# Performance work log

Measured on AMD Instinct MI355X. Metric: run time of the kernel, lower is better.

Reference implementation:

```python
import jax, jax.numpy as jnp
import numpy as np

D = 768
H = 12
HD = D // H
EPS = 1e-8  # torch cosine_similarity default eps


def setup_inputs() -> dict:
    key = jax.random.key(0)
    ks = jax.random.split(key, 16)
    bs, T, K = 8, 2048, 512
    s = 0.02
    return {
        "hidden_states": jax.random.normal(ks[0], (bs, T, D), jnp.float32),
        "attention_mask": jnp.ones((bs, T), jnp.int32),
        "pooled_hidden_states": jax.random.normal(ks[1], (bs, D), jnp.float32),
        "kg_key": jax.random.normal(ks[2], (bs, K, D), jnp.float32),
        "kg_value": jax.random.normal(ks[3], (bs, K, D), jnp.float32),
        "beta": jnp.ones((H,), jnp.float32),
        "Wq": jax.random.normal(ks[4], (D, D), jnp.float32) * s,
        "bq": jnp.zeros((D,), jnp.float32),
        "Wk": jax.random.normal(ks[5], (D, D), jnp.float32) * s,
        "bk": jnp.zeros((D,), jnp.float32),
        "Wv": jax.random.normal(ks[6], (D, D), jnp.float32) * s,
        "bv": jnp.zeros((D,), jnp.float32),
        "Wo": jax.random.normal(ks[7], (D, D), jnp.float32) * s,
        "bo": jnp.zeros((D,), jnp.float32),
    }


def reference(hidden_states, attention_mask, pooled_hidden_states, kg_key, kg_value,
              beta, Wq, bq, Wk, bk, Wv, bv, Wo, bo):
    bs, T, _ = hidden_states.shape
    K = kg_key.shape[1]
    # cosine similarity between pooled state and each KG key: [bs, K]
    pn = pooled_hidden_states / jnp.maximum(
        jnp.linalg.norm(pooled_hidden_states, axis=-1, keepdims=True), EPS)
    kn = kg_key / jnp.maximum(jnp.linalg.norm(kg_key, axis=-1, keepdims=True), EPS)
    sim = jnp.einsum("bd,bkd->bk", pn, kn)

    scale = HD ** -0.5
    # projections (torch Linear: y = x @ W.T + b)
    q = ((hidden_states @ Wq.T + bq) * scale).reshape(bs, T, H, HD).transpose(0, 2, 1, 3)
    k = (kg_value @ Wk.T + bk).reshape(bs, K, H, HD).transpose(0, 2, 1, 3)
    v = (kg_value @ Wv.T + bv).reshape(bs, K, H, HD).transpose(0, 2, 1, 3)

    # scores + per-head cosine-sim bias: [bs, H, T, K]
    scores = jnp.einsum("bhtd,bhkd->bhtk", q, k)
    scores = scores + beta[None, :, None, None] * sim[:, None, None, :]
    probs = jax.nn.softmax(scores, axis=-1)

    out = jnp.einsum("bhtk,bhkd->bhtd", probs, v)
    out = out.transpose(0, 2, 1, 3).reshape(bs, T, D)
    return out @ Wo.T + bo
```

## Files before the change

kernel.cpp:

```cpp
#include <hip/hip_runtime.h>
#include <math.h>

#define D_MODEL 768
#define NHEAD   12
#define HD      64
#define SEQ_T   2048
#define SEQ_K   512
#define BS      8
#define EPS_COS 1e-8f
#define LOG2E   1.44269504f

typedef short  bf16x8 __attribute__((ext_vector_type(8)));
typedef float  f32x4  __attribute__((ext_vector_type(4)));

__device__ __forceinline__ ushort f2bf(float x) {
    unsigned b = __float_as_uint(x);
    return (ushort)((b + 0x7FFF + ((b >> 16) & 1)) >> 16);
}
__device__ __forceinline__ unsigned cvt_pk_bf16(float lo, float hi) {
    unsigned r;
    asm("v_cvt_pk_bf16_f32 %0, %1, %2" : "=v"(r) : "v"(lo), "v"(hi));
    return r;
}
__device__ __forceinline__ float exp2_fast(float x) {
    float r;
    asm("v_exp_f32 %0, %1" : "=v"(r) : "v"(x));
    return r;
}

__device__ __forceinline__ void async_copy16(void* lds_base, const void* g_src) {
    __builtin_amdgcn_global_load_lds(
        (const __attribute__((address_space(1))) unsigned int*)g_src,
        (__attribute__((address_space(3))) unsigned int*)lds_base,
        16, 0, 0);
}

__global__ __launch_bounds__(256) void cvt4_kernel(
    const float* __restrict__ s0, const float* __restrict__ s1,
    const float* __restrict__ s2, const float* __restrict__ s3,
    ushort* __restrict__ d0, ushort* __restrict__ d1,
    ushort* __restrict__ d2, ushort* __restrict__ d3)
{
    const float* s; ushort* d;
    switch (blockIdx.y) {
        case 0: s = s0; d = d0; break;
        case 1: s = s1; d = d1; break;
        case 2: s = s2; d = d2; break;
        default: s = s3; d = d3; break;
    }
    int i = blockIdx.x * 256 + threadIdx.x;
    float4 v = reinterpret_cast<const float4*>(s)[i];
    ushort4 o;
    o.x = f2bf(v.x); o.y = f2bf(v.y); o.z = f2bf(v.z); o.w = f2bf(v.w);
    reinterpret_cast<ushort4*>(d)[i] = o;
}

__global__ __launch_bounds__(256) void sim_kernel(
    const float* __restrict__ pooled, const float* __restrict__ kg_key,
    const float* __restrict__ beta, float* __restrict__ bsim)
{
    int wid  = (blockIdx.x * blockDim.x + threadIdx.x) >> 6;
    int lane = threadIdx.x & 63;
    int b  = wid >> 9;
    int kk = wid & 511;
    const float* p   = pooled + (size_t)b * D_MODEL;
    const float* key = kg_key + ((size_t)b * SEQ_K + kk) * D_MODEL;
    float dpk = 0.f, dkk = 0.f, dpp = 0.f;
    for (int i = lane; i < D_MODEL; i += 64) {
        float pv = p[i], kv = key[i];
        dpk += pv * kv; dkk += kv * kv; dpp += pv * pv;
    }
    for (int off = 32; off; off >>= 1) {
        dpk += __shfl_xor(dpk, off);
        dkk += __shfl_xor(dkk, off);
        dpp += __shfl_xor(dpp, off);
    }
    if (lane == 0) {
        float np_ = fmaxf(sqrtf(dpp), EPS_COS);
        float nk_ = fmaxf(sqrtf(dkk), EPS_COS);
        float sv = (dpk / (np_ * nk_)) * LOG2E;
#pragma unroll
        for (int h = 0; h < NHEAD; ++h)
            bsim[(size_t)(b * NHEAD + h) * SEQ_K + kk] = beta[h] * sv;
    }
}

__global__ __launch_bounds__(256, 3) void gemm_q_a32_kernel(
    const float* __restrict__ A, const ushort* __restrict__ W,
    const float* __restrict__ bias, ushort* __restrict__ out_bf, float scale)
{
    constexpr int Kd = D_MODEL;
    __shared__ __align__(16) float  AsF[128 * 64];
    __shared__ __align__(16) ushort Bs[128 * 64];
    const int tid = threadIdx.x, wid = tid >> 6, l = tid & 63;
    const int g = l >> 4, c = l & 15;
    const int m0 = blockIdx.x * 128, n0 = blockIdx.y * 128;
    const int wm = (wid >> 1) * 64, wn = (wid & 1) * 64;

    f32x4 acc[4][4] = {};

    for (int k0 = 0; k0 < Kd; k0 += 64) {
        __syncthreads();
#pragma unroll
        for (int it = 0; it < 8; ++it) {
            int L = wid * 8192 + it * 1024 + l * 16;
            int row = L >> 8;
            int blk = (L >> 4) & 15;
            int gb = (blk & 8) | ((blk & 7) ^ (row & 7));
            async_copy16((char*)AsF + wid * 8192 + it * 1024,
                         A + (size_t)(m0 + row) * Kd + k0 + gb * 4);
        }
#pragma unroll
        for (int it = 0; it < 4; ++it) {
            int L = wid * 4096 + it * 1024 + l * 16;
            int row = L >> 7;
            int gb = ((L >> 4) & 7) ^ (row & 7);
            async_copy16((char*)Bs + wid * 4096 + it * 1024,
                         W + (size_t)(n0 + row) * Kd + k0 + gb * 8);
        }
        __syncthreads();

        bf16x8 af[4][2], bf[4][2];
#pragma unroll
        for (int mt = 0; mt < 4; ++mt)
#pragma unroll
            for (int ks = 0; ks < 2; ++ks) {
                int row = wm + mt * 16 + c;
                int b0 = ks * 8 + 2 * g;
                int p0 = (b0 & 8) | ((b0 & 7) ^ (row & 7));
                int p1 = (b0 & 8) | (((b0 + 1) & 7) ^ (row & 7));
                f32x4 a0 = *(const f32x4*)((const char*)AsF + row * 256 + (p0 << 4));
                f32x4 a1 = *(const f32x4*)((const char*)AsF + row * 256 + (p1 << 4));
                union { unsigned u[4]; bf16x8 v; } t;
                t.u[0] = cvt_pk_bf16(a0[0], a0[1]);
                t.u[1] = cvt_pk_bf16(a0[2], a0[3]);
                t.u[2] = cvt_pk_bf16(a1[0], a1[1]);
                t.u[3] = cvt_pk_bf16(a1[2], a1[3]);
                af[mt][ks] = t.v;
            }
#pragma unroll
        for (int nt = 0; nt < 4; ++nt)
#pragma unroll
            for (int ks = 0; ks < 2; ++ks) {
                int row = wn + nt * 16 + c;
                bf[nt][ks] = *(const bf16x8*)((const char*)Bs + row * 128 +
                                              (((ks * 4 + g) ^ (row & 7)) << 4));
            }
        __builtin_amdgcn_s_setprio(1);
#pragma unroll
        for (int mt = 0; mt < 4; ++mt)
#pragma unroll
            for (int nt = 0; nt < 4; ++nt) {
                acc[mt][nt] = __builtin_amdgcn_mfma_f32_16x16x32_bf16(
                    af[mt][0], bf[nt][0], acc[mt][nt], 0, 0, 0);
                acc[mt][nt] = __builtin_amdgcn_mfma_f32_16x16x32_bf16(
                    af[mt][1], bf[nt][1], acc[mt][nt], 0, 0, 0);
            }
        __builtin_amdgcn_s_setprio(0);
    }

#pragma unroll
    for (int mt = 0; mt < 4; ++mt)
#pragma unroll
        for (int nt = 0; nt < 4; ++nt) {
            int col = n0 + wn + nt * 16 + c;
            float bv = bias[col];
#pragma unroll
            for (int j = 0; j < 4; ++j) {
                int row = m0 + wm + mt * 16 + g * 4 + j;
                out_bf[(size_t)row * Kd + col] = f2bf((acc[mt][nt][j] + bv) * scale);
            }
        }
}

__global__ __launch_bounds__(256, 3) void gemm_kv_a32_kernel(
    const float* __restrict__ A,
    const ushort* __restrict__ Wk_, const float* __restrict__ bk_,
    const ushort* __restrict__ Wv_, const float* __restrict__ bv_,
    ushort* __restrict__ outk, ushort* __restrict__ vt)
{
    constexpr int Kd = D_MODEL;
    __shared__ __align__(16) float  AsF[64 * 64];
    __shared__ __align__(16) ushort Bk[64 * 64];
    __shared__ __align__(16) ushort Bv[64 * 64];
    const int tid = threadIdx.x, wid = tid >> 6, l = tid & 63;
    const int g = l >> 4, c = l & 15;
    const int m0 = blockIdx.x * 64, h = blockIdx.y, n0 = h * 64;
    const int wm = (wid >> 1) * 32, wn = (wid & 1) * 32;

    f32x4 acck[2][2] = {}, accv[2][2] = {};

    for (int k0 = 0; k0 < Kd; k0 += 64) {
        __syncthreads();
#pragma unroll
        for (int it = 0; it < 4; ++it) {
            int L = wid * 4096 + it * 1024 + l * 16;
            int row = L >> 8;
            int blk = (L >> 4) & 15;
            int gb = (blk & 8) | ((blk & 7) ^ (row & 7));
            async_copy16((char*)AsF + wid * 4096 + it * 1024,
                         A + (size_t)(m0 + row) * Kd + k0 + gb * 4);
        }
#pragma unroll
        for (int it = 0; it < 2; ++it) {
            int L = wid * 2048 + it * 1024 + l * 16;
            int row = L >> 7;
            int gb = ((L >> 4) & 7) ^ (row & 7);
            async_copy16((char*)Bk + wid * 2048 + it * 1024,
                         Wk_ + (size_t)(n0 + row) * Kd + k0 + gb * 8);
            async_copy16((char*)Bv + wid * 2048 + it * 1024,
                         Wv_ + (size_t)(n0 + row) * Kd + k0 + gb * 8);
        }
        __syncthreads();

        bf16x8 af[2][2], bkf[2][2], bvf[2][2];
#pragma unroll
        for (int mt = 0; mt < 2; ++mt)
#pragma unroll
            for (int ks = 0; ks < 2; ++ks) {
                int row = wm + mt * 16 + c;
                int b0 = ks * 8 + 2 * g;
                int p0 = (b0 & 8) | ((b0 & 7) ^ (row & 7));
                int p1 = (b0 & 8) | (((b0 + 1) & 7) ^ (row & 7));
                f32x4 a0 = *(const f32x4*)((const char*)AsF + row * 256 + (p0 << 4));
                f32x4 a1 = *(const f32x4*)((const char*)AsF + row * 256 + (p1 << 4));
                union { unsigned u[4]; bf16x8 v; } t;
                t.u[0] = cvt_pk_bf16(a0[0], a0[1]);
                t.u[1] = cvt_pk_bf16(a0[2], a0[3]);
                t.u[2] = cvt_pk_bf16(a1[0], a1[1]);
                t.u[3] = cvt_pk_bf16(a1[2], a1[3]);
                af[mt][ks] = t.v;
            }
#pragma unroll
        for (int nt = 0; nt < 2; ++nt)
#pragma unroll
            for (int ks = 0; ks < 2; ++ks) {
                int row = wn + nt * 16 + c;
                int off = row * 128 + (((ks * 4 + g) ^ (row & 7)) << 4);
                bkf[nt][ks] = *(const bf16x8*)((const char*)Bk + off);
                bvf[nt][ks] = *(const bf16x8*)((const char*)Bv + off);
            }
        __builtin_amdgcn_s_setprio(1);
#pragma unroll
        for (int mt = 0; mt < 2; ++mt)
#pragma unroll
            for (int nt = 0; nt < 2; ++nt)
#pragma unroll
                for (int ks = 0; ks < 2; ++ks) {
                    acck[mt][nt] = __builtin_amdgcn_mfma_f32_16x16x32_bf16(
                        af[mt][ks], bkf[nt][ks], acck[mt][nt], 0, 0, 0);
                    accv[mt][nt] = __builtin_amdgcn_mfma_f32_16x16x32_bf16(
                        af[mt][ks], bvf[nt][ks], accv[mt][nt], 0, 0, 0);
                }
        __builtin_amdgcn_s_setprio(0);
    }

#pragma unroll
    for (int mt = 0; mt < 2; ++mt)
#pragma unroll
        for (int nt = 0; nt < 2; ++nt) {
            int col = n0 + wn + nt * 16 + c;
            float bbk = bk_[col];
#pragma unroll
            for (int j = 0; j < 4; ++j) {
                int row = m0 + wm + mt * 16 + 4 * g + j;
                outk[(size_t)row * Kd + col] = f2bf(acck[mt][nt][j] + bbk);
            }
        }

    {
        int b = m0 >> 9;
        int kc = (m0 >> 7) & 3;
#pragma unroll
        for (int mt = 0; mt < 2; ++mt) {
            int kb0 = (m0 & 64) + wm + mt * 16 + 4 * g;
            int kp0 = ((kb0 >> 5) << 5) | (((kb0 >> 2) & 3) << 3) | (((kb0 >> 4) & 1) << 2);
#pragma unroll
            for (int nt = 0; nt < 2; ++nt) {
                int d = wn + nt * 16 + c;
                float bbv = bv_[n0 + d];
                unsigned u0 = cvt_pk_bf16(accv[mt][nt][0] + bbv, accv[mt][nt][1] + bbv);
                unsigned u1 = cvt_pk_bf16(accv[mt][nt][2] + bbv, accv[mt][nt][3] + bbv);
                size_t base = ((size_t)(b * NHEAD + h) * HD + d) * SEQ_K + kc * 128 + kp0;
                uint2 st2; st2.x = u0; st2.y = u1;
                *(uint2*)(vt + base) = st2;
            }
        }
    }
}

__global__ __launch_bounds__(256, 2) void gemm_o_kernel(
    const ushort* __restrict__ A, const ushort* __restrict__ W,
    const float* __restrict__ bias, float* __restrict__ out_f32)
{
    constexpr int Kd = D_MODEL;
    __shared__ __align__(16) ushort As[128 * 64];
    __shared__ __align__(16) ushort Bs[128 * 64];
    const int tid = threadIdx.x, wid = tid >> 6, l = tid & 63;
    const int g = l >> 4, c = l & 15;
    const int m0 = blockIdx.x * 128, n0 = blockIdx.y * 128;
    const int wm = (wid >> 1) * 64, wn = (wid & 1) * 64;

    f32x4 acc[4][4] = {};

    for (int k0 = 0; k0 < Kd; k0 += 64) {
        __syncthreads();
#pragma unroll
        for (int it = 0; it < 4; ++it) {
            int L = wid * 4096 + it * 1024 + l * 16;
            int row = L >> 7;
            int gb = ((L >> 4) & 7) ^ (row & 7);
            async_copy16((char*)As + wid * 4096 + it * 1024,
                         A + (size_t)(m0 + row) * Kd + k0 + gb * 8);
        }
#pragma unroll
        for (int it = 0; it < 4; ++it) {
            int L = wid * 4096 + it * 1024 + l * 16;
            int row = L >> 7;
            int gb = ((L >> 4) & 7) ^ (row & 7);
            async_copy16((char*)Bs + wid * 4096 + it * 1024,
                         W + (size_t)(n0 + row) * Kd + k0 + gb * 8);
        }
        __syncthreads();

        bf16x8 af[4][2], bf[4][2];
#pragma unroll
        for (int mt = 0; mt < 4; ++mt)
#pragma unroll
            for (int ks = 0; ks < 2; ++ks) {
                int row = wm + mt * 16 + c;
                af[mt][ks] = *(const bf16x8*)((const char*)As + row * 128 +
                                              (((ks * 4 + g) ^ (row & 7)) << 4));
            }
#pragma unroll
        for (int nt = 0; nt < 4; ++nt)
#pragma unroll
            for (int ks = 0; ks < 2; ++ks) {
                int row = wn + nt * 16 + c;
                bf[nt][ks] = *(const bf16x8*)((const char*)Bs + row * 128 +
                                              (((ks * 4 + g) ^ (row & 7)) << 4));
            }
        __builtin_amdgcn_s_setprio(1);
#pragma unroll
        for (int mt = 0; mt < 4; ++mt)
#pragma unroll
            for (int nt = 0; nt < 4; ++nt) {
                acc[mt][nt] = __builtin_amdgcn_mfma_f32_16x16x32_bf16(
                    af[mt][0], bf[nt][0], acc[mt][nt], 0, 0, 0);
                acc[mt][nt] = __builtin_amdgcn_mfma_f32_16x16x32_bf16(
                    af[mt][1], bf[nt][1], acc[mt][nt], 0, 0, 0);
            }
        __builtin_amdgcn_s_setprio(0);
    }

#pragma unroll
    for (int mt = 0; mt < 4; ++mt)
#pragma unroll
        for (int nt = 0; nt < 4; ++nt) {
            int col = n0 + wn + nt * 16 + c;
            float bv = bias[col];
#pragma unroll
            for (int j = 0; j < 4; ++j) {
                int row = m0 + wm + mt * 16 + g * 4 + j;
                out_f32[(size_t)row * Kd + col] = acc[mt][nt][j] + bv;
            }
        }
}

__global__ __launch_bounds__(256, 2) void attn_mfma_kernel(
    const ushort* __restrict__ qb, const ushort* __restrict__ kbp,
    const ushort* __restrict__ vt, const float* __restrict__ bsim,
    ushort* __restrict__ ctx)
{
    int bid = blockIdx.x;
    int w = (bid & 7) * 96 + (bid >> 3);
    int tile = w & 7; int rest = w >> 3; int h = rest % 12; int b = rest / 12;
    int t0 = tile * 256;
    int tid = threadIdx.x, wid = tid >> 6, l = tid & 63;
    int g = l >> 4, c = l & 15;

    __shared__ __align__(16) ushort KV[2][128 * 128];

    const ushort* srck[4]; const ushort* srcv[4];
    int offk[4], offv[4];
#pragma unroll
    for (int it = 0; it < 4; ++it) {
        int L = wid * 4096 + it * 1024 + l * 16;
        int row = L >> 7;
        int gb = ((L >> 4) & 7) ^ (row & 7);
        srck[it] = kbp + (size_t)(b * SEQ_K + row) * D_MODEL + h * HD + gb * 8;
        offk[it] = wid * 4096 + it * 1024;
        int d = L >> 8;
        int blk = (L >> 4) & 15;
        int gblk = (blk & 8) | ((blk & 7) ^ (d & 7));
        srcv[it] = vt + ((size_t)((b * NHEAD + h) * HD + d)) * SEQ_K + gblk * 8;
        offv[it] = 16384 + wid * 4096 + it * 1024;
    }

#pragma unroll
    for (int it = 0; it < 8; ++it) {
        int L = wid * 8192 + it * 1024 + l * 16;
        int row = L >> 7;
        int gb = ((L >> 4) & 7) ^ (row & 7);
        async_copy16((char*)KV[0] + wid * 8192 + it * 1024,
                     qb + (size_t)(b * SEQ_T + t0 + row) * D_MODEL + h * HD + gb * 8);
    }
    const float* bsrow = bsim + (size_t)(b * NHEAD + h) * SEQ_K;
    __syncthreads();

    bf16x8 aq[4][2];
#pragma unroll
    for (int sub = 0; sub < 4; ++sub)
#pragma unroll
        for (int ks = 0; ks < 2; ++ks) {
            int row = wid * 64 + sub * 16 + c;
            aq[sub][ks] = *(const bf16x8*)((const char*)KV[0] + row * 128 +
                                           (((ks * 4 + g) ^ (row & 7)) << 4));
        }
    __syncthreads();

#pragma unroll
    for (int it = 0; it < 4; ++it) {
        async_copy16((char*)KV[0] + offk[it], srck[it]);
        async_copy16((char*)KV[0] + offv[it], srcv[it]);
    }

    const bf16x8 ones8 = {(short)0x3F80, (short)0x3F80, (short)0x3F80, (short)0x3F80,
                          (short)0x3F80, (short)0x3F80, (short)0x3F80, (short)0x3F80};
    f32x4 oacc[4][4] = {};
    f32x4 oSum[4] = {};
    int cur = 0;

    for (int kc = 0; kc < 4; ++kc) {
        __syncthreads();
        if (kc < 3) {
            int nxt = cur ^ 1;
#pragma unroll
            for (int it = 0; it < 4; ++it) {
                srck[it] += 128 * D_MODEL;
                async_copy16((char*)KV[nxt] + offk[it], srck[it]);
                srcv[it] += 128;
                async_copy16((char*)KV[nxt] + offv[it], srcv[it]);
            }
        }
        const char* Kb = (const char*)KV[cur];
        const char* Vb = (const char*)KV[cur] + 16384;

#pragma unroll
        for (int kb = 0; kb < 4; ++kb) {
            f32x4 st[4][2];
            __builtin_amdgcn_s_setprio(1);
#pragma unroll
            for (int n2 = 0; n2 < 2; ++n2) {
                int nt = 2 * kb + n2;
                f32x4 cinit = *(const f32x4*)(bsrow + kc * 128 + nt * 16 + 4 * g);
                int krow = nt * 16 + c;
                bf16x8 ak0 = *(const bf16x8*)(Kb + krow * 128 +
                                              ((g ^ (krow & 7)) << 4));
                bf16x8 ak1 = *(const bf16x8*)(Kb + krow * 128 +
                                              (((4 + g) ^ (krow & 7)) << 4));
#pragma unroll
                for (int sub = 0; sub < 4; ++sub) {
                    st[sub][n2] = __builtin_amdgcn_mfma_f32_16x16x32_bf16(
                        ak0, aq[sub][0], cinit, 0, 0, 0);
                    st[sub][n2] = __builtin_amdgcn_mfma_f32_16x16x32_bf16(
                        ak1, aq[sub][1], st[sub][n2], 0, 0, 0);
                }
            }
            __builtin_amdgcn_s_setprio(0);

            bf16x8 pa[4];
#pragma unroll
            for (int sub = 0; sub < 4; ++sub) {
                f32x4 e0, e1;
#pragma unroll
                for (int j = 0; j < 4; ++j) {
                    e0[j] = exp2_fast(st[sub][0][j]);
                    e1[j] = exp2_fast(st[sub][1][j]);
                }
                union { unsigned u[4]; bf16x8 v; } pk;
                pk.u[0] = cvt_pk_bf16(e0[0], e0[1]);
                pk.u[1] = cvt_pk_bf16(e0[2], e0[3]);
                pk.u[2] = cvt_pk_bf16(e1[0], e1[1]);
                pk.u[3] = cvt_pk_bf16(e1[2], e1[3]);
                pa[sub] = pk.v;
            }

            __builtin_amdgcn_s_setprio(1);
#pragma unroll
            for (int sub = 0; sub < 4; ++sub)
                oSum[sub] = __builtin_amdgcn_mfma_f32_16x16x32_bf16(
                    pa[sub], ones8, oSum[sub], 0, 0, 0);
#pragma unroll
            for (int dt = 0; dt < 4; ++dt) {
                int d = dt * 16 + c;
                int blk = kb * 4 + g;
                int sb = (blk & 8) | ((blk & 7) ^ (d & 7));
                bf16x8 bv = *(const bf16x8*)(Vb + d * 256 + sb * 16);
#pragma unroll
                for (int sub = 0; sub < 4; ++sub)
                    oacc[sub][dt] = __builtin_amdgcn_mfma_f32_16x16x32_bf16(
                        pa[sub], bv, oacc[sub][dt], 0, 0, 0);
            }
            __builtin_amdgcn_s_setprio(0);
        }
        cur ^= 1;
    }

#pragma unroll
    for (int sub = 0; sub < 4; ++sub) {
        f32x4 invL;
#pragma unroll
        for (int j = 0; j < 4; ++j) invL[j] = 1.f / oSum[sub][j];
#pragma unroll
        for (int dt = 0; dt < 4; ++dt)
#pragma unroll
            for (int j = 0; j < 4; ++j) {
                int trow = t0 + wid * 64 + sub * 16 + 4 * g + j;
                int d = dt * 16 + c;
                ctx[(size_t)(b * SEQ_T + trow) * D_MODEL + h * HD + d] =
                    f2bf(oacc[sub][dt][j] * invL[j]);
            }
    }
}

extern "C" void kernel_launch(void* const* d_in, const int* in_sizes, int n_in,
                              void* d_out, int out_size, void* d_ws, size_t ws_size,
                              hipStream_t stream)
{
    const float* hidden  = (const float*)d_in[0];
    const float* pooled  = (const float*)d_in[2];
    const float* kg_key  = (const float*)d_in[3];
    const float* kg_val  = (const float*)d_in[4];
    const float* beta    = (const float*)d_in[5];
    const float* Wq = (const float*)d_in[6];  const float* bq = (const float*)d_in[7];
    const float* Wk = (const float*)d_in[8];  const float* bk = (const float*)d_in[9];
    const float* Wv = (const float*)d_in[10]; const float* bv = (const float*)d_in[11];
    const float* Wo = (const float*)d_in[12]; const float* bo = (const float*)d_in[13];
    float* out = (float*)d_out;

    const size_t MQ = (size_t)BS * SEQ_T;
    const size_t MK = (size_t)BS * SEQ_K;
    const size_t DW = D_MODEL * D_MODEL;

    float*  bsim = (float*)d_ws;
    ushort* wqb  = (ushort*)(bsim + BS * NHEAD * SEQ_K);
    ushort* wkb  = wqb + DW;
    ushort* wvb  = wkb + DW;
    ushort* wob  = wvb + DW;
    ushort* qbb  = wob + DW;
    ushort* kbb  = qbb + MQ * D_MODEL;
    ushort* vtb  = kbb + MK * D_MODEL;
    ushort* ctxb = vtb + MK * D_MODEL;

    cvt4_kernel<<<dim3(DW / 4 / 256, 4), 256, 0, stream>>>(
        Wq, Wk, Wv, Wo, wqb, wkb, wvb, wob);

    sim_kernel<<<(BS * SEQ_K) / 4, 256, 0, stream>>>(pooled, kg_key, beta, bsim);

    gemm_q_a32_kernel<<<dim3(MQ / 128, 6), 256, 0, stream>>>(
        hidden, wqb, bq, qbb, 0.125f * LOG2E);
    gemm_kv_a32_kernel<<<dim3(MK / 64, 12), 256, 0, stream>>>(
        kg_val, wkb, bk, wvb, bv, kbb, vtb);

    attn_mfma_kernel<<<BS * NHEAD * (SEQ_T / 256), 256, 0, stream>>>(
        qbb, kbb, vtb, bsim, ctxb);

    gemm_o_kernel<<<dim3(MQ / 128, 6), 256, 0, stream>>>(ctxb, wob, bo, out);
}
```

Baseline: 126.0 us.

## Fuse Q/KV projections and cosine-sim into one launch; shrink attention tiles

Merges the Q projection GEMM, the K/V projection GEMM and the cosine-similarity kernel into one launch that picks its role from the block index, so three launches become one and the independent work can share the GPU. The attention kernel now uses 128-row query tiles and 64-key chunks with smaller LDS buffers, and sets launch bounds for 4 blocks per CU to double the grid and raise occupancy. In exchange, each attention block reloads K/V twice as often overall, and the fused kernel's register and LDS use is set by its heaviest branch.

```diff
diff --git a/kernel.cpp b/kernel.cpp
--- a/kernel.cpp
+++ b/kernel.cpp
@@ -55,236 +55,228 @@
     reinterpret_cast<ushort4*>(d)[i] = o;
 }
 
-__global__ __launch_bounds__(256) void sim_kernel(
+__global__ __launch_bounds__(256, 3) void fused_proj_sim_kernel(
+    const float* __restrict__ hidden, const float* __restrict__ kg_val,
+    const ushort* __restrict__ Wqb, const float* __restrict__ bq,
+    const ushort* __restrict__ Wkb, const float* __restrict__ bk_,
+    const ushort* __restrict__ Wvb, const float* __restrict__ bv_,
     const float* __restrict__ pooled, const float* __restrict__ kg_key,
-    const float* __restrict__ beta, float* __restrict__ bsim)
+    const float* __restrict__ beta,
+    ushort* __restrict__ qout, ushort* __restrict__ kout,
+    ushort* __restrict__ vtout, float* __restrict__ bsim, float qscale)
 {
-    int wid  = (blockIdx.x * blockDim.x + threadIdx.x) >> 6;
-    int lane = threadIdx.x & 63;
-    int b  = wid >> 9;
-    int kk = wid & 511;
-    const float* p   = pooled + (size_t)b * D_MODEL;
-    const float* key = kg_key + ((size_t)b * SEQ_K + kk) * D_MODEL;
-    float dpk = 0.f, dkk = 0.f, dpp = 0.f;
-    for (int i = lane; i < D_MODEL; i += 64) {
-        float pv = p[i], kv = key[i];
-        dpk += pv * kv; dkk += kv * kv; dpp += pv * pv;
-    }
-    for (int off = 32; off; off >>= 1) {
-        dpk += __shfl_xor(dpk, off);
-        dkk += __shfl_xor(dkk, off);
-        dpp += __shfl_xor(dpp, off);
-    }
-    if (lane == 0) {
-        float np_ = fmaxf(sqrtf(dpp), EPS_COS);
-        float nk_ = fmaxf(sqrtf(dkk), EPS_COS);
-        float sv = (dpk / (np_ * nk_)) * LOG2E;
-#pragma unroll
-        for (int h = 0; h < NHEAD; ++h)
-            bsim[(size_t)(b * NHEAD + h) * SEQ_K + kk] = beta[h] * sv;
-    }
-}
-
-__global__ __launch_bounds__(256, 3) void gemm_q_a32_kernel(
-    const float* __restrict__ A, const ushort* __restrict__ W,
-    const float* __restrict__ bias, ushort* __restrict__ out_bf, float scale)
-{
+    __shared__ __align__(16) char lds[49152];
     constexpr int Kd = D_MODEL;
-    __shared__ __align__(16) float  AsF[128 * 64];
-    __shared__ __align__(16) ushort Bs[128 * 64];
+    const int bid = blockIdx.x;
     const int tid = threadIdx.x, wid = tid >> 6, l = tid & 63;
     const int g = l >> 4, c = l & 15;
-    const int m0 = blockIdx.x * 128, n0 = blockIdx.y * 128;
-    const int wm = (wid >> 1) * 64, wn = (wid & 1) * 64;
-
-    f32x4 acc[4][4] = {};
-
-    for (int k0 = 0; k0 < Kd; k0 += 64) {
-        __syncthreads();
-#pragma unroll
-        for (int it = 0; it < 8; ++it) {
-            int L = wid * 8192 + it * 1024 + l * 16;
-            int row = L >> 8;
-            int blk = (L >> 4) & 15;
-            int gb = (blk & 8) | ((blk & 7) ^ (row & 7));
-            async_copy16((char*)AsF + wid * 8192 + it * 1024,
-                         A + (size_t)(m0 + row) * Kd + k0 + gb * 4);
-        }
-#pragma unroll
-        for (int it = 0; it < 4; ++it) {
-            int L = wid * 4096 + it * 1024 + l * 16;
-            int row = L >> 7;
-            int gb = ((L >> 4) & 7) ^ (row & 7);
-            async_copy16((char*)Bs + wid * 4096 + it * 1024,
-                         W + (size_t)(n0 + row) * Kd + k0 + gb * 8);
-        }
-        __syncthreads();
-
-        bf16x8 af[4][2], bf[4][2];
+
+    if (bid < 768) {
+        float*  AsF = (float*)lds;
+        ushort* Bs  = (ushort*)(lds + 32768);
+        const int m0 = (bid & 127) * 128, n0 = (bid >> 7) * 128;
+        const int wm = (wid >> 1) * 64, wn = (wid & 1) * 64;
+
+        f32x4 acc[4][4] = {};
+        for (int k0 = 0; k0 < Kd; k0 += 64) {
+            __syncthreads();
+#pragma unroll
+            for (int it = 0; it < 8; ++it) {
+                int L = wid * 8192 + it * 1024 + l * 16;
+                int row = L >> 8;
+                int blk = (L >> 4) & 15;
+                int gb = (blk & 8) | ((blk & 7) ^ (row & 7));
+                async_copy16((char*)AsF + wid * 8192 + it * 1024,
+                             hidden + (size_t)(m0 + row) * Kd + k0 + gb * 4);
+            }
+#pragma unroll
+            for (int it = 0; it < 4; ++it) {
+                int L = wid * 4096 + it * 1024 + l * 16;
+                int row = L >> 7;
+                int gb = ((L >> 4) & 7) ^ (row & 7);
+                async_copy16((char*)Bs + wid * 4096 + it * 1024,
+                             Wqb + (size_t)(n0 + row) * Kd + k0 + gb * 8);
+            }
+            __syncthreads();
+
+            bf16x8 af[4][2], bf[4][2];
+#pragma unroll
+            for (int mt = 0; mt < 4; ++mt)
+#pragma unroll
+                for (int ks = 0; ks < 2; ++ks) {
+                    int row = wm + mt * 16 + c;
+                    int b0 = ks * 8 + 2 * g;
+                    int p0 = (b0 & 8) | ((b0 & 7) ^ (row & 7));
+                    int p1 = (b0 & 8) | (((b0 + 1) & 7) ^ (row & 7));
+                    f32x4 a0 = *(const f32x4*)((const char*)AsF + row * 256 + (p0 << 4));
+                    f32x4 a1 = *(const f32x4*)((const char*)AsF + row * 256 + (p1 << 4));
+                    union { unsigned u[4]; bf16x8 v; } t;
+                    t.u[0] = cvt_pk_bf16(a0[0], a0[1]);
+                    t.u[1] = cvt_pk_bf16(a0[2], a0[3]);
+                    t.u[2] = cvt_pk_bf16(a1[0], a1[1]);
+                    t.u[3] = cvt_pk_bf16(a1[2], a1[3]);
+                    af[mt][ks] = t.v;
+                }
+#pragma unroll
+            for (int nt = 0; nt < 4; ++nt)
+#pragma unroll
+                for (int ks = 0; ks < 2; ++ks) {
+                    int row = wn + nt * 16 + c;
+                    bf[nt][ks] = *(const bf16x8*)((const char*)Bs + row * 128 +
+                                                  (((ks * 4 + g) ^ (row & 7)) << 4));
+                }
+            __builtin_amdgcn_s_setprio(1);
+#pragma unroll
+            for (int mt = 0; mt < 4; ++mt)
+#pragma unroll
+                for (int nt = 0; nt < 4; ++nt) {
+                    acc[mt][nt] = __builtin_amdgcn_mfma_f32_16x16x32_bf16(
+                        af[mt][0], bf[nt][0], acc[mt][nt], 0, 0, 0);
+                    acc[mt][nt] = __builtin_amdgcn_mfma_f32_16x16x32_bf16(
+                        af[mt][1], bf[nt][1], acc[mt][nt], 0, 0, 0);
+                }
+            __builtin_amdgcn_s_setprio(0);
+        }
 #pragma unroll
         for (int mt = 0; mt < 4; ++mt)
 #pragma unroll
-            for (int ks = 0; ks < 2; ++ks) {
-                int row = wm + mt * 16 + c;
-                int b0 = ks * 8 + 2 * g;
-                int p0 = (b0 & 8) | ((b0 & 7) ^ (row & 7));
-                int p1 = (b0 & 8) | (((b0 + 1) & 7) ^ (row & 7));
-                f32x4 a0 = *(const f32x4*)((const char*)AsF + row * 256 + (p0 << 4));
-                f32x4 a1 = *(const f32x4*)((const char*)AsF + row * 256 + (p1 << 4));
-                union { unsigned u[4]; bf16x8 v; } t;
-                t.u[0] = cvt_pk_bf16(a0[0], a0[1]);
-                t.u[1] = cvt_pk_bf16(a0[2], a0[3]);
-                t.u[2] = cvt_pk_bf16(a1[0], a1[1]);
-                t.u[3] = cvt_pk_bf16(a1[2], a1[3]);
-                af[mt][ks] = t.v;
-            }
-#pragma unroll
-        for (int nt = 0; nt < 4; ++nt)
-#pragma unroll
-            for (int ks = 0; ks < 2; ++ks) {
-                int row = wn + nt * 16 + c;
-                bf[nt][ks] = *(const bf16x8*)((const char*)Bs + row * 128 +
-                                              (((ks * 4 + g) ^ (row & 7)) << 4));
-            }
-        __builtin_amdgcn_s_setprio(1);
-#pragma unroll
-        for (int mt = 0; mt < 4; ++mt)
-#pragma unroll
             for (int nt = 0; nt < 4; ++nt) {
-                acc[mt][nt] = __builtin_amdgcn_mfma_f32_16x16x32_bf16(
-                    af[mt][0], bf[nt][0], acc[mt][nt], 0, 0, 0);
-                acc[mt][nt] = __builtin_amdgcn_mfma_f32_16x16x32_bf16(
-                    af[mt][1], bf[nt][1], acc[mt][nt], 0, 0, 0);
-            }
-        __builtin_amdgcn_s_setprio(0);
-    }
-
-#pragma unroll
-    for (int mt = 0; mt < 4; ++mt)
-#pragma unroll
-        for (int nt = 0; nt < 4; ++nt) {
-            int col = n0 + wn + nt * 16 + c;
-            float bv = bias[col];
-#pragma unroll
-            for (int j = 0; j < 4; ++j) {
-                int row = m0 + wm + mt * 16 + g * 4 + j;
-                out_bf[(size_t)row * Kd + col] = f2bf((acc[mt][nt][j] + bv) * scale);
-            }
-        }
-}
-
-__global__ __launch_bounds__(256, 3) void gemm_kv_a32_kernel(
-    const float* __restrict__ A,
-    const ushort* __restrict__ Wk_, const float* __restrict__ bk_,
-    const ushort* __restrict__ Wv_, const float* __restrict__ bv_,
-    ushort* __restrict__ outk, ushort* __restrict__ vt)
-{
-    constexpr int Kd = D_MODEL;
-    __shared__ __align__(16) float  AsF[64 * 64];
-    __shared__ __align__(16) ushort Bk[64 * 64];
-    __shared__ __align__(16) ushort Bv[64 * 64];
-    const int tid = threadIdx.x, wid = tid >> 6, l = tid & 63;
-    const int g = l >> 4, c = l & 15;
-    const int m0 = blockIdx.x * 64, h = blockIdx.y, n0 = h * 64;
-    const int wm = (wid >> 1) * 32, wn = (wid & 1) * 32;
-
-    f32x4 acck[2][2] = {}, accv[2][2] = {};
-
-    for (int k0 = 0; k0 < Kd; k0 += 64) {
-        __syncthreads();
-#pragma unroll
-        for (int it = 0; it < 4; ++it) {
-            int L = wid * 4096 + it * 1024 + l * 16;
-            int row = L >> 8;
-            int blk = (L >> 4) & 15;
-            int gb = (blk & 8) | ((blk & 7) ^ (row & 7));
-            async_copy16((char*)AsF + wid * 4096 + it * 1024,
-                         A + (size_t)(m0 + row) * Kd + k0 + gb * 4);
-        }
-#pragma unroll
-        for (int it = 0; it < 2; ++it) {
-            int L = wid * 2048 + it * 1024 + l * 16;
-            int row = L >> 7;
-            int gb = ((L >> 4) & 7) ^ (row & 7);
-            async_copy16((char*)Bk + wid * 2048 + it * 1024,
-                         Wk_ + (size_t)(n0 + row) * Kd + k0 + gb * 8);
-            async_copy16((char*)Bv + wid * 2048 + it * 1024,
-                         Wv_ + (size_t)(n0 + row) * Kd + k0 + gb * 8);
-        }
-        __syncthreads();
-
-        bf16x8 af[2][2], bkf[2][2], bvf[2][2];
+                int col = n0 + wn + nt * 16 + c;
+                float bv = bq[col];
+#pragma unroll
+                for (int j = 0; j < 4; ++j) {
+                    int row = m0 + wm + mt * 16 + g * 4 + j;
+                    qout[(size_t)row * Kd + col] = f2bf((acc[mt][nt][j] + bv) * qscale);
+                }
+            }
+    } else if (bid < 1536) {
+        float*  AsF = (float*)lds;
+        ushort* Bk  = (ushort*)(lds + 16384);
+        ushort* Bv  = (ushort*)(lds + 24576);
+        const int q = bid - 768;
+        const int m0 = (q & 63) * 64, h = q >> 6, n0 = h * 64;
+        const int wm = (wid >> 1) * 32, wn = (wid & 1) * 32;
+
+        f32x4 acck[2][2] = {}, accv[2][2] = {};
+        for (int k0 = 0; k0 < Kd; k0 += 64) {
+            __syncthreads();
+#pragma unroll
+            for (int it = 0; it < 4; ++it) {
+                int L = wid * 4096 + it * 1024 + l * 16;
+                int row = L >> 8;
+                int blk = (L >> 4) & 15;
+                int gb = (blk & 8) | ((blk & 7) ^ (row & 7));
+                async_copy16((char*)AsF + wid * 4096 + it * 1024,
+                             kg_val + (size_t)(m0 + row) * Kd + k0 + gb * 4);
+            }
+#pragma unroll
+            for (int it = 0; it < 2; ++it) {
+                int L = wid * 2048 + it * 1024 + l * 16;
+                int row = L >> 7;
+                int gb = ((L >> 4) & 7) ^ (row & 7);
+                async_copy16((char*)Bk + wid * 2048 + it * 1024,
+                             Wkb + (size_t)(n0 + row) * Kd + k0 + gb * 8);
+                async_copy16((char*)Bv + wid * 2048 + it * 1024,
+                             Wvb + (size_t)(n0 + row) * Kd + k0 + gb * 8);
+            }
+            __syncthreads();
+
+            bf16x8 af[2][2], bkf[2][2], bvf[2][2];
+#pragma unroll
+            for (int mt = 0; mt < 2; ++mt)
+#pragma unroll
+                for (int ks = 0; ks < 2; ++ks) {
+                    int row = wm + mt * 16 + c;
+                    int b0 = ks * 8 + 2 * g;
+                    int p0 = (b0 & 8) | ((b0 & 7) ^ (row & 7));
+                    int p1 = (b0 & 8) | (((b0 + 1) & 7) ^ (row & 7));
+                    f32x4 a0 = *(const f32x4*)((const char*)AsF + row * 256 + (p0 << 4));
+                    f32x4 a1 = *(const f32x4*)((const char*)AsF + row * 256 + (p1 << 4));
+                    union { unsigned u[4]; bf16x8 v; } t;
+                    t.u[0] = cvt_pk_bf16(a0[0], a0[1]);
+                    t.u[1] = cvt_pk_bf16(a0[2], a0[3]);
+                    t.u[2] = cvt_pk_bf16(a1[0], a1[1]);
+                    t.u[3] = cvt_pk_bf16(a1[2], a1[3]);
+                    af[mt][ks] = t.v;
+                }
+#pragma unroll
+            for (int nt = 0; nt < 2; ++nt)
+#pragma unroll
+                for (int ks = 0; ks < 2; ++ks) {
+                    int row = wn + nt * 16 + c;
+                    int off = row * 128 + (((ks * 4 + g) ^ (row & 7)) << 4);
+                    bkf[nt][ks] = *(const bf16x8*)((const char*)Bk + off);
+                    bvf[nt][ks] = *(const bf16x8*)((const char*)Bv + off);
+                }
+            __builtin_amdgcn_s_setprio(1);
+#pragma unroll
+            for (int mt = 0; mt < 2; ++mt)
+#pragma unroll
+                for (int nt = 0; nt < 2; ++nt)
+#pragma unroll
+                    for (int ks = 0; ks < 2; ++ks) {
+                        acck[mt][nt] = __builtin_amdgcn_mfma_f32_16x16x32_bf16(
+                            af[mt][ks], bkf[nt][ks], acck[mt][nt], 0, 0, 0);
+                        accv[mt][nt] = __builtin_amdgcn_mfma_f32_16x16x32_bf16(
+                            af[mt][ks], bvf[nt][ks], accv[mt][nt], 0, 0, 0);
+                    }
+            __builtin_amdgcn_s_setprio(0);
+        }
 #pragma unroll
         for (int mt = 0; mt < 2; ++mt)
 #pragma unroll
-            for (int ks = 0; ks < 2; ++ks) {
-                int row = wm + mt * 16 + c;
-                int b0 = ks * 8 + 2 * g;
-                int p0 = (b0 & 8) | ((b0 & 7) ^ (row & 7));
-                int p1 = (b0 & 8) | (((b0 + 1) & 7) ^ (row & 7));
-                f32x4 a0 = *(const f32x4*)((const char*)AsF + row * 256 + (p0 << 4));
-                f32x4 a1 = *(const f32x4*)((const char*)AsF + row * 256 + (p1 << 4));
-                union { unsigned u[4]; bf16x8 v; } t;
-                t.u[0] = cvt_pk_bf16(a0[0], a0[1]);
-                t.u[1] = cvt_pk_bf16(a0[2], a0[3]);
-                t.u[2] = cvt_pk_bf16(a1[0], a1[1]);
-                t.u[3] = cvt_pk_bf16(a1[2], a1[3]);
-                af[mt][ks] = t.v;
-            }
-#pragma unroll
-        for (int nt = 0; nt < 2; ++nt)
-#pragma unroll
-            for (int ks = 0; ks < 2; ++ks) {
-                int row = wn + nt * 16 + c;
-                int off = row * 128 + (((ks * 4 + g) ^ (row & 7)) << 4);
-                bkf[nt][ks] = *(const bf16x8*)((const char*)Bk + off);
-                bvf[nt][ks] = *(const bf16x8*)((const char*)Bv + off);
-            }
-        __builtin_amdgcn_s_setprio(1);
-#pragma unroll
-        for (int mt = 0; mt < 2; ++mt)
-#pragma unroll
-            for (int nt = 0; nt < 2; ++nt)
-#pragma unroll
-                for (int ks = 0; ks < 2; ++ks) {
-                    acck[mt][nt] = __builtin_amdgcn_mfma_f32_16x16x32_bf16(
-                        af[mt][ks], bkf[nt][ks], acck[mt][nt], 0, 0, 0);
-                    accv[mt][nt] = __builtin_amdgcn_mfma_f32_16x16x32_bf16(
-                        af[mt][ks], bvf[nt][ks], accv[mt][nt], 0, 0, 0);
-                }
-        __builtin_amdgcn_s_setprio(0);
-    }
-
-#pragma unroll
-    for (int mt = 0; mt < 2; ++mt)
-#pragma unroll
-        for (int nt = 0; nt < 2; ++nt) {
-            int col = n0 + wn + nt * 16 + c;
-            float bbk = bk_[col];
-#pragma unroll
-            for (int j = 0; j < 4; ++j) {
-                int row = m0 + wm + mt * 16 + 4 * g + j;
-                outk[(size_t)row * Kd + col] = f2bf(acck[mt][nt][j] + bbk);
-            }
-        }
-
-    {
-        int b = m0 >> 9;
-        int kc = (m0 >> 7) & 3;
-#pragma unroll
-        for (int mt = 0; mt < 2; ++mt) {
-            int kb0 = (m0 & 64) + wm + mt * 16 + 4 * g;
-            int kp0 = ((kb0 >> 5) << 5) | (((kb0 >> 2) & 3) << 3) | (((kb0 >> 4) & 1) << 2);
-#pragma unroll
             for (int nt = 0; nt < 2; ++nt) {
-                int d = wn + nt * 16 + c;
-                float bbv = bv_[n0 + d];
-                unsigned u0 = cvt_pk_bf16(accv[mt][nt][0] + bbv, accv[mt][nt][1] + bbv);
-                unsigned u1 = cvt_pk_bf16(accv[mt][nt][2] + bbv, accv[mt][nt][3] + bbv);
-                size_t base = ((size_t)(b * NHEAD + h) * HD + d) * SEQ_K + kc * 128 + kp0;
-                uint2 st2; st2.x = u0; st2.y = u1;
-                *(uint2*)(vt + base) = st2;
-            }
+                int col = n0 + wn + nt * 16 + c;
+                float bbk = bk_[col];
+#pragma unroll
+                for (int j = 0; j < 4; ++j) {
+                    int row = m0 + wm + mt * 16 + 4 * g + j;
+                    kout[(size_t)row * Kd + col] = f2bf(acck[mt][nt][j] + bbk);
+                }
+            }
+        {
+            int b = m0 >> 9;
+            int kc = (m0 >> 7) & 3;
+#pragma unroll
+            for (int mt = 0; mt < 2; ++mt) {
+                int kb0 = (m0 & 64) + wm + mt * 16 + 4 * g;
+                int kp0 = ((kb0 >> 5) << 5) | (((kb0 >> 2) & 3) << 3) | (((kb0 >> 4) & 1) << 2);
+#pragma unroll
+                for (int nt = 0; nt < 2; ++nt) {
+                    int d = wn + nt * 16 + c;
+                    float bbv = bv_[n0 + d];
+                    unsigned u0 = cvt_pk_bf16(accv[mt][nt][0] + bbv, accv[mt][nt][1] + bbv);
+                    unsigned u1 = cvt_pk_bf16(accv[mt][nt][2] + bbv, accv[mt][nt][3] + bbv);
+                    size_t base = ((size_t)(b * NHEAD + h) * HD + d) * SEQ_K + kc * 128 + kp0;
+                    uint2 st2; st2.x = u0; st2.y = u1;
+                    *(uint2*)(vtout + base) = st2;
+                }
+            }
+        }
+    } else {
+        int wrow = (bid - 1536) * 4 + (tid >> 6);
+        int lane = tid & 63;
+        int b  = wrow >> 9;
+        int kk = wrow & 511;
+        const float* p   = pooled + (size_t)b * D_MODEL;
+        const float* key = kg_key + ((size_t)b * SEQ_K + kk) * D_MODEL;
+        float dpk = 0.f, dkk = 0.f, dpp = 0.f;
+        for (int i = lane; i < D_MODEL; i += 64) {
+            float pv = p[i], kv = key[i];
+            dpk += pv * kv; dkk += kv * kv; dpp += pv * pv;
+        }
+        for (int off = 32; off; off >>= 1) {
+            dpk += __shfl_xor(dpk, off);
+            dkk += __shfl_xor(dkk, off);
+            dpp += __shfl_xor(dpp, off);
+        }
+        if (lane == 0) {
+            float np_ = fmaxf(sqrtf(dpp), EPS_COS);
+            float nk_ = fmaxf(sqrtf(dkk), EPS_COS);
+            float sv = (dpk / (np_ * nk_)) * LOG2E;
+#pragma unroll
+            for (int h = 0; h < NHEAD; ++h)
+                bsim[(size_t)(b * NHEAD + h) * SEQ_K + kk] = beta[h] * sv;
         }
     }
 }
@@ -367,100 +359,100 @@
         }
 }
 
-__global__ __launch_bounds__(256, 2) void attn_mfma_kernel(
+__global__ __launch_bounds__(256, 4) void attn_mfma_kernel(
     const ushort* __restrict__ qb, const ushort* __restrict__ kbp,
     const ushort* __restrict__ vt, const float* __restrict__ bsim,
     ushort* __restrict__ ctx)
 {
     int bid = blockIdx.x;
-    int w = (bid & 7) * 96 + (bid >> 3);
-    int tile = w & 7; int rest = w >> 3; int h = rest % 12; int b = rest / 12;
-    int t0 = tile * 256;
+    int w = (bid & 7) * 192 + (bid >> 3);
+    int tile = w & 15; int rest = w >> 4; int h = rest % 12; int b = rest / 12;
+    int t0 = tile * 128;
     int tid = threadIdx.x, wid = tid >> 6, l = tid & 63;
     int g = l >> 4, c = l & 15;
 
-    __shared__ __align__(16) ushort KV[2][128 * 128];
-
-    const ushort* srck[4]; const ushort* srcv[4];
-    int offk[4], offv[4];
+    __shared__ __align__(16) char KV[2][16384];
+
+    const ushort* srck[2]; const ushort* srcv[2];
+    int offk[2], offv[2];
+#pragma unroll
+    for (int it = 0; it < 2; ++it) {
+        int L = wid * 2048 + it * 1024 + l * 16;
+        int row = L >> 7;
+        int gb = ((L >> 4) & 7) ^ (row & 7);
+        srck[it] = kbp + (size_t)(b * SEQ_K + row) * D_MODEL + h * HD + gb * 8;
+        offk[it] = wid * 2048 + it * 1024;
+        int d = row;
+        int blk = (L >> 4) & 7;
+        int gblk = blk ^ (d & 7);
+        srcv[it] = vt + ((size_t)((b * NHEAD + h) * HD + d)) * SEQ_K + gblk * 8;
+        offv[it] = 8192 + wid * 2048 + it * 1024;
+    }
+
 #pragma unroll
     for (int it = 0; it < 4; ++it) {
         int L = wid * 4096 + it * 1024 + l * 16;
         int row = L >> 7;
         int gb = ((L >> 4) & 7) ^ (row & 7);
-        srck[it] = kbp + (size_t)(b * SEQ_K + row) * D_MODEL + h * HD + gb * 8;
-        offk[it] = wid * 4096 + it * 1024;
-        int d = L >> 8;
-        int blk = (L >> 4) & 15;
-        int gblk = (blk & 8) | ((blk & 7) ^ (d & 7));
-        srcv[it] = vt + ((size_t)((b * NHEAD + h) * HD + d)) * SEQ_K + gblk * 8;
-        offv[it] = 16384 + wid * 4096 + it * 1024;
-    }
-
-#pragma unroll
-    for (int it = 0; it < 8; ++it) {
-        int L = wid * 8192 + it * 1024 + l * 16;
-        int row = L >> 7;
-        int gb = ((L >> 4) & 7) ^ (row & 7);
-        async_copy16((char*)KV[0] + wid * 8192 + it * 1024,
+        async_copy16(&KV[0][0] + wid * 4096 + it * 1024,
                      qb + (size_t)(b * SEQ_T + t0 + row) * D_MODEL + h * HD + gb * 8);
     }
     const float* bsrow = bsim + (size_t)(b * NHEAD + h) * SEQ_K;
     __syncthreads();
 
-    bf16x8 aq[4][2];
-#pragma unroll
-    for (int sub = 0; sub < 4; ++sub)
+    bf16x8 aq[2][2];
+#pragma unroll
+    for (int sub = 0; sub < 2; ++sub)
 #pragma unroll
         for (int ks = 0; ks < 2; ++ks) {
-            int row = wid * 64 + sub * 16 + c;
-            aq[sub][ks] = *(const bf16x8*)((const char*)KV[0] + row * 128 +
+            int row = wid * 32 + sub * 16 + c;
+            aq[sub][ks] = *(const bf16x8*)(&KV[0][0] + row * 128 +
                                            (((ks * 4 + g) ^ (row & 7)) << 4));
         }
     __syncthreads();
 
 #pragma unroll
-    for (int it = 0; it < 4; ++it) {
-        async_copy16((char*)KV[0] + offk[it], srck[it]);
-        async_copy16((char*)KV[0] + offv[it], srcv[it]);
+    for (int it = 0; it < 2; ++it) {
+        async_copy16(&KV[0][0] + offk[it], srck[it]);
+        async_copy16(&KV[0][0] + offv[it], srcv[it]);
     }
 
     const bf16x8 ones8 = {(short)0x3F80, (short)0x3F80, (short)0x3F80, (short)0x3F80,
                           (short)0x3F80, (short)0x3F80, (short)0x3F80, (short)0x3F80};
-    f32x4 oacc[4][4] = {};
-    f32x4 oSum[4] = {};
+    f32x4 oacc[2][4] = {};
+    f32x4 oSum[2] = {};
     int cur = 0;
 
-    for (int kc = 0; kc < 4; ++kc) {
+    for (int kc = 0; kc < 8; ++kc) {
         __syncthreads();
-        if (kc < 3) {
+        if (kc < 7) {
             int nxt = cur ^ 1;
 #pragma unroll
-            for (int it = 0; it < 4; ++it) {
-                srck[it] += 128 * D_MODEL;
-                async_copy16((char*)KV[nxt] + offk[it], srck[it]);
-                srcv[it] += 128;
-                async_copy16((char*)KV[nxt] + offv[it], srcv[it]);
-            }
-        }
-        const char* Kb = (const char*)KV[cur];
-        const char* Vb = (const char*)KV[cur] + 16384;
-
-#pragma unroll
-        for (int kb = 0; kb < 4; ++kb) {
-            f32x4 st[4][2];
+            for (int it = 0; it < 2; ++it) {
+                srck[it] += 64 * D_MODEL;
+                async_copy16(&KV[nxt][0] + offk[it], srck[it]);
+                srcv[it] += 64;
+                async_copy16(&KV[nxt][0] + offv[it], srcv[it]);
+            }
+        }
+        const char* Kb = &KV[cur][0];
+        const char* Vb = &KV[cur][0] + 8192;
+
+#pragma unroll
+        for (int kb = 0; kb < 2; ++kb) {
+            f32x4 st[2][2];
             __builtin_amdgcn_s_setprio(1);
 #pragma unroll
             for (int n2 = 0; n2 < 2; ++n2) {
                 int nt = 2 * kb + n2;
-                f32x4 cinit = *(const f32x4*)(bsrow + kc * 128 + nt * 16 + 4 * g);
+                f32x4 cinit = *(const f32x4*)(bsrow + kc * 64 + nt * 16 + 4 * g);
                 int krow = nt * 16 + c;
                 bf16x8 ak0 = *(const bf16x8*)(Kb + krow * 128 +
                                               ((g ^ (krow & 7)) << 4));
                 bf16x8 ak1 = *(const bf16x8*)(Kb + krow * 128 +
                                               (((4 + g) ^ (krow & 7)) << 4));
 #pragma unroll
-                for (int sub = 0; sub < 4; ++sub) {
+                for (int sub = 0; sub < 2; ++sub) {
                     st[sub][n2] = __builtin_amdgcn_mfma_f32_16x16x32_bf16(
                         ak0, aq[sub][0], cinit, 0, 0, 0);
                     st[sub][n2] = __builtin_amdgcn_mfma_f32_16x16x32_bf16(
@@ -469,9 +461,9 @@
             }
             __builtin_amdgcn_s_setprio(0);
 
-            bf16x8 pa[4];
-#pragma unroll
-            for (int sub = 0; sub < 4; ++sub) {
+            bf16x8 pa[2];
+#pragma unroll
+            for (int sub = 0; sub < 2; ++sub) {
                 f32x4 e0, e1;
 #pragma unroll
                 for (int j = 0; j < 4; ++j) {
@@ -488,17 +480,17 @@
 
             __builtin_amdgcn_s_setprio(1);
 #pragma unroll
-            for (int sub = 0; sub < 4; ++sub)
+            for (int sub = 0; sub < 2; ++sub)
                 oSum[sub] = __builtin_amdgcn_mfma_f32_16x16x32_bf16(
                     pa[sub], ones8, oSum[sub], 0, 0, 0);
 #pragma unroll
             for (int dt = 0; dt < 4; ++dt) {
                 int d = dt * 16 + c;
                 int blk = kb * 4 + g;
-                int sb = (blk & 8) | ((blk & 7) ^ (d & 7));
-                bf16x8 bv = *(const bf16x8*)(Vb + d * 256 + sb * 16);
-#pragma unroll
-                for (int sub = 0; sub < 4; ++sub)
+                int sb = blk ^ (d & 7);
+                bf16x8 bv = *(const bf16x8*)(Vb + d * 128 + (sb << 4));
+#pragma unroll
+                for (int sub = 0; sub < 2; ++sub)
                     oacc[sub][dt] = __builtin_amdgcn_mfma_f32_16x16x32_bf16(
                         pa[sub], bv, oacc[sub][dt], 0, 0, 0);
             }
@@ -508,7 +500,7 @@
     }
 
 #pragma unroll
-    for (int sub = 0; sub < 4; ++sub) {
+    for (int sub = 0; sub < 2; ++sub) {
         f32x4 invL;
 #pragma unroll
         for (int j = 0; j < 4; ++j) invL[j] = 1.f / oSum[sub][j];
@@ -516,7 +508,7 @@
         for (int dt = 0; dt < 4; ++dt)
 #pragma unroll
             for (int j = 0; j < 4; ++j) {
-                int trow = t0 + wid * 64 + sub * 16 + 4 * g + j;
+                int trow = t0 + wid * 32 + sub * 16 + 4 * g + j;
                 int d = dt * 16 + c;
                 ctx[(size_t)(b * SEQ_T + trow) * D_MODEL + h * HD + d] =
                     f2bf(oacc[sub][dt][j] * invL[j]);
@@ -556,14 +548,11 @@
     cvt4_kernel<<<dim3(DW / 4 / 256, 4), 256, 0, stream>>>(
         Wq, Wk, Wv, Wo, wqb, wkb, wvb, wob);
 
-    sim_kernel<<<(BS * SEQ_K) / 4, 256, 0, stream>>>(pooled, kg_key, beta, bsim);
-
-    gemm_q_a32_kernel<<<dim3(MQ / 128, 6), 256, 0, stream>>>(
-        hidden, wqb, bq, qbb, 0.125f * LOG2E);
-    gemm_kv_a32_kernel<<<dim3(MK / 64, 12), 256, 0, stream>>>(
-        kg_val, wkb, bk, wvb, bv, kbb, vtb);
-
-    attn_mfma_kernel<<<BS * NHEAD * (SEQ_T / 256), 256, 0, stream>>>(
+    fused_proj_sim_kernel<<<2560, 256, 0, stream>>>(
+        hidden, kg_val, wqb, bq, wkb, bk, wvb, bv,
+        pooled, kg_key, beta, qbb, kbb, vtb, bsim, 0.125f * LOG2E);
+
+    attn_mfma_kernel<<<BS * NHEAD * (SEQ_T / 128), 256, 0, stream>>>(
         qbb, kbb, vtb, bsim, ctxb);
 
     gemm_o_kernel<<<dim3(MQ / 128, 6), 256, 0, stream>>>(ctxb, wob, bo, out);
```

After: 118.3 us. 1.06x faster.
